# Optimization experiments

Measured on AMD Instinct MI355X. Metric: run time of the kernel, lower is better.

The kernel has to match this reference:

```python
import jax, jax.numpy as jnp
import numpy as np

B, NQ, NC, D, H, HD, FF, RB = 2, 512, 2048, 768, 12, 64, 3072, 64
EPS = 1e-5


def setup_inputs() -> dict:
    key = jax.random.key(0)
    ks = jax.random.split(key, 20)
    def n(k, shape, s=0.02):
        return jax.random.normal(k, shape, jnp.float32) * s
    return dict(
        query_state=n(ks[0], (B, NQ, D), 1.0),
        context_k=n(ks[1], (B, NC, D), 1.0),
        context_v=n(ks[2], (B, NC, D), 1.0),
        query_coords=jax.random.uniform(ks[3], (B, NQ, 2), jnp.float32),
        context_coords=jax.random.uniform(ks[4], (B, NC, 2), jnp.float32),
        sn_g=jnp.ones(D), sn_b=jnp.zeros(D),
        wqkv=n(ks[5], (D, 3 * D)), bqkv=jnp.zeros(3 * D),
        wo_s=n(ks[6], (D, D)), bo_s=jnp.zeros(D),
        cn_g=jnp.ones(D), cn_b=jnp.zeros(D),
        wq=n(ks[7], (D, D)), bq=jnp.zeros(D),
        wk=n(ks[8], (D, D)), bk=jnp.zeros(D),
        wv=n(ks[9], (D, D)), bv=jnp.zeros(D),
        wo_c=n(ks[10], (D, D)), bo_c=jnp.zeros(D),
        rb_w1=n(ks[11], (2, RB), 0.5), rb_b1=jnp.zeros(RB),
        rb_w2=n(ks[12], (RB, H), 0.5), rb_b2=jnp.zeros(H),
        fn_g=jnp.ones(D), fn_b=jnp.zeros(D),
        fw1=n(ks[13], (D, FF)), fb1=jnp.zeros(FF),
        fw2=n(ks[14], (FF, D)), fb2=jnp.zeros(D),
    )


def _ln(x, g, b):
    m = x.mean(-1, keepdims=True)
    v = ((x - m) ** 2).mean(-1, keepdims=True)
    return (x - m) / jnp.sqrt(v + EPS) * g + b


def _heads(x):
    # (B, N, D) -> (B, H, N, HD)
    return x.reshape(x.shape[0], x.shape[1], H, HD).transpose(0, 2, 1, 3)


def reference(query_state, context_k, context_v, query_coords, context_coords,
              sn_g, sn_b, wqkv, bqkv, wo_s, bo_s,
              cn_g, cn_b, wq, bq, wk, bk, wv, bv, wo_c, bo_c,
              rb_w1, rb_b1, rb_w2, rb_b2,
              fn_g, fn_b, fw1, fb1, fw2, fb2):
    scale = HD ** -0.5
    x = query_state

    # ---- pre-norm self-attention (nn.MultiheadAttention equivalent) ----
    qn = _ln(x, sn_g, sn_b)
    qkv = qn @ wqkv + bqkv                      # (B, NQ, 3D)
    q, k, v = jnp.split(qkv, 3, axis=-1)
    q, k, v = _heads(q), _heads(k), _heads(v)   # (B, H, NQ, HD)
    a = jax.nn.softmax(jnp.einsum('bhqd,bhkd->bhqk', q, k) * scale, axis=-1)
    o = jnp.einsum('bhqk,bhkd->bhqd', a, v).transpose(0, 2, 1, 3).reshape(B, NQ, D)
    x = x + o @ wo_s + bo_s

    # ---- relative coordinate bias: MLP(delta) -> (B, H, NQ, NC) ----
    delta = query_coords[:, :, None, :] - context_coords[:, None, :, :]  # (B, NQ, NC, 2)
    bias = jax.nn.gelu(delta @ rb_w1 + rb_b1, approximate=False) @ rb_w2 + rb_b2
    bias = bias.transpose(0, 3, 1, 2)           # (B, H, NQ, NC)

    # ---- pre-norm cross-attention with bias ----
    qn = _ln(x, cn_g, cn_b)
    q = _heads(qn @ wq + bq)                    # (B, H, NQ, HD)
    k = _heads(context_k @ wk + bk)             # (B, H, NC, HD)
    v = _heads(context_v @ wv + bv)
    logits = jnp.einsum('bhqd,bhkd->bhqk', q, k) * scale + bias
    a = jax.nn.softmax(logits, axis=-1)
    o = jnp.einsum('bhqk,bhkd->bhqd', a, v).transpose(0, 2, 1, 3).reshape(B, NQ, D)
    x = x + o @ wo_c + bo_c

    # ---- pre-norm FFN ----
    h = jax.nn.gelu(_ln(x, fn_g, fn_b) @ fw1 + fb1, approximate=False)
    x = x + h @ fw2 + fb2
    return x
```

## Files before the change

kernel.cpp:

```cpp
#include <hip/hip_runtime.h>

#define B_ 2
#define NQ_ 512
#define NC_ 2048
#define D_ 768
#define H_ 12
#define HD_ 64
#define FF_ 3072
#define RB_ 64

typedef unsigned short u16;
typedef __attribute__((ext_vector_type(4))) unsigned short u16x4;
typedef __attribute__((ext_vector_type(8))) short short8;
typedef __attribute__((ext_vector_type(4))) float f32x4;
typedef __attribute__((ext_vector_type(2))) float f32x2;

__device__ __forceinline__ float bf2f(u16 u) {
    unsigned int i = ((unsigned int)u) << 16;
    float f; __builtin_memcpy(&f, &i, 4); return f;
}
__device__ __forceinline__ u16 f2bf(float f) {
    unsigned int i; __builtin_memcpy(&i, &f, 4);
    unsigned int r = i + 0x7FFFu + ((i >> 16) & 1u);
    return (u16)(r >> 16);
}
__device__ __forceinline__ float gelu_f(float x) {
    return 0.5f * x * (1.f + erff(x * 0.70710678118654752f));
}
__device__ __forceinline__ float wsum(float v) {
    v += __shfl_xor(v, 32); v += __shfl_xor(v, 16); v += __shfl_xor(v, 8);
    v += __shfl_xor(v, 4);  v += __shfl_xor(v, 2);  v += __shfl_xor(v, 1);
    return v;
}
__device__ __forceinline__ void gload_lds16(const void* g, void* l) {
    __builtin_amdgcn_global_load_lds((const __attribute__((address_space(1))) void*)g,
                                     (__attribute__((address_space(3))) void*)l, 16, 0, 0);
}

__device__ __forceinline__ void wtrans_body(const float* __restrict__ in, u16* __restrict__ out,
                                            int K, int N, int bx, int by, int tid) {
    __shared__ float t[32][33];
    int n0 = bx * 32, k0 = by * 32;
    int tx = tid & 31, ty = tid >> 5;
#pragma unroll
    for (int r = 0; r < 4; ++r)
        t[ty + r * 8][tx] = in[(long)(k0 + ty + r * 8) * N + n0 + tx];
    __syncthreads();
#pragma unroll
    for (int r = 0; r < 4; ++r)
        out[(long)(n0 + ty + r * 8) * K + k0 + tx] = f2bf(t[tx][ty + r * 8]);
}

__global__ __launch_bounds__(256) void wtrans(const float* __restrict__ in, u16* __restrict__ out,
                                              int K, int N) {
    wtrans_body(in, out, K, N, blockIdx.x, blockIdx.y, threadIdx.x);
}

__global__ __launch_bounds__(256) void wtrans5(const float* i0, const float* i1, const float* i2,
                                               const float* i3, const float* i4,
                                               u16* o0, u16* o1, u16* o2, u16* o3, u16* o4) {
    const float* in; u16* out;
    switch (blockIdx.z) {
        case 0: in = i0; out = o0; break;
        case 1: in = i1; out = o1; break;
        case 2: in = i2; out = o2; break;
        case 3: in = i3; out = o3; break;
        default: in = i4; out = o4; break;
    }
    wtrans_body(in, out, 768, 768, blockIdx.x, blockIdx.y, threadIdx.x);
}

__global__ __launch_bounds__(256) void cvtk2(const float* __restrict__ inA, u16* __restrict__ outA,
                                             const float* __restrict__ inB, u16* __restrict__ outB, int n4) {
    int i = blockIdx.x * 256 + threadIdx.x;
    const float* in = blockIdx.y ? inB : inA;
    u16* out = blockIdx.y ? outB : outA;
    if (i < n4) {
        float4 v = ((const float4*)in)[i];
        u16x4 o; o.x = f2bf(v.x); o.y = f2bf(v.y); o.z = f2bf(v.z); o.w = f2bf(v.w);
        ((u16x4*)out)[i] = o;
    }
}

__global__ __launch_bounds__(256) void ln_k(const float* __restrict__ x, const float* __restrict__ g,
                                            const float* __restrict__ bta, u16* __restrict__ out) {
    int row = blockIdx.x, t = threadIdx.x;
    const float* xr = x + (long)row * D_;
    float a0 = xr[t], a1 = xr[t + 256], a2 = xr[t + 512];
    float s = a0 + a1 + a2, s2 = a0 * a0 + a1 * a1 + a2 * a2;
    s = wsum(s); s2 = wsum(s2);
    __shared__ float rb[8];
    int lane = t & 63, wid = t >> 6;
    if (!lane) { rb[wid] = s; rb[wid + 4] = s2; }
    __syncthreads();
    float S = rb[0] + rb[1] + rb[2] + rb[3];
    float S2 = rb[4] + rb[5] + rb[6] + rb[7];
    float mean = S * (1.f / D_);
    float var = S2 * (1.f / D_) - mean * mean;
    float rstd = rsqrtf(var + 1e-5f);
    u16* orow = out + (long)row * D_;
    orow[t]       = f2bf((a0 - mean) * rstd * g[t]       + bta[t]);
    orow[t + 256] = f2bf((a1 - mean) * rstd * g[t + 256] + bta[t + 256]);
    orow[t + 512] = f2bf((a2 - mean) * rstd * g[t + 512] + bta[t + 512]);
}

__global__ __launch_bounds__(256) void bias_mlp3(
    const float* __restrict__ qcoord, const float* __restrict__ ccoord,
    const float* __restrict__ w1, const float* __restrict__ b1,
    const float* __restrict__ w2, const float* __restrict__ b2,
    u16* __restrict__ out) {
    __shared__ float s1[192];
    __shared__ float sw2[RB_ * H_];
    __shared__ float2 sc[256];
    __shared__ u16 sb[12 * 264];
    int tid = threadIdx.x;
    int b = blockIdx.z, q = blockIdx.y, c0 = blockIdx.x * 256;
    if (tid < 64) { s1[tid] = w1[tid]; s1[64 + tid] = w1[64 + tid]; s1[128 + tid] = b1[tid]; }
    for (int i = tid; i < RB_ * H_; i += 256) sw2[i] = w2[i];
    sc[tid] = ((const float2*)ccoord)[b * NC_ + c0 + tid];
    __syncthreads();
    int lane = tid & 63, wid = tid >> 6;
    int h = lane & 15, g4 = lane >> 4;
    int j0 = g4 * 8;
    f32x2 wx[8], wy[8], bb[8];
#pragma unroll
    for (int p = 0; p < 4; ++p) {
        wx[p]     = (f32x2){s1[j0 + 2 * p],       s1[j0 + 2 * p + 1]};
        wy[p]     = (f32x2){s1[64 + j0 + 2 * p],  s1[64 + j0 + 2 * p + 1]};
        bb[p]     = (f32x2){s1[128 + j0 + 2 * p], s1[128 + j0 + 2 * p + 1]};
        wx[4 + p] = (f32x2){s1[32 + j0 + 2 * p],  s1[32 + j0 + 2 * p + 1]};
        wy[4 + p] = (f32x2){s1[96 + j0 + 2 * p],  s1[96 + j0 + 2 * p + 1]};
        bb[4 + p] = (f32x2){s1[160 + j0 + 2 * p], s1[160 + j0 + 2 * p + 1]};
    }
    short8 vb0, vb1;
#pragma unroll
    for (int u = 0; u < 8; ++u) {
        vb0[u] = (h < 12) ? (short)f2bf(sw2[(j0 + u) * H_ + h]) : (short)0;
        vb1[u] = (h < 12) ? (short)f2bf(sw2[(32 + j0 + u) * H_ + h]) : (short)0;
    }
    float qx = qcoord[(b * NQ_ + q) * 2], qy = qcoord[(b * NQ_ + q) * 2 + 1];
    float b2v = (h < 12) ? b2[h] : 0.f;
#pragma unroll
    for (int it = 0; it < 4; ++it) {
        int ci = wid * 64 + it * 16 + h;
        float2 cc = sc[ci];
        float dx = qx - cc.x, dy = qy - cc.y;
        unsigned int pk[8];
#pragma unroll
        for (int p = 0; p < 8; ++p) {
            f32x2 pre = dx * wx[p] + bb[p];
            pre = dy * wy[p] + pre;
            f32x2 t = pre * pre;
            f32x2 a = 1.5957691f + 0.07135482f * t;
            f32x2 uu = pre * a;
            f32x2 e; e.x = __expf(uu.x); e.y = __expf(uu.y);
            e = e + 1.0f;
            f32x2 r; r.x = __builtin_amdgcn_rcpf(e.x); r.y = __builtin_amdgcn_rcpf(e.y);
            f32x2 g = pre - pre * r;
            pk[p] = __builtin_amdgcn_perm(__builtin_bit_cast(unsigned int, g.y),
                                          __builtin_bit_cast(unsigned int, g.x), 0x07060302u);
        }
        uint4 d0 = {pk[0], pk[1], pk[2], pk[3]};
        uint4 d1 = {pk[4], pk[5], pk[6], pk[7]};
        short8 a0 = __builtin_bit_cast(short8, d0);
        short8 a1 = __builtin_bit_cast(short8, d1);
        f32x4 acc = {};
        acc = __builtin_amdgcn_mfma_f32_16x16x32_bf16(a0, vb0, acc, 0, 0, 0);
        acc = __builtin_amdgcn_mfma_f32_16x16x32_bf16(a1, vb1, acc, 0, 0, 0);
        if (h < 12) {
#pragma unroll
            for (int r = 0; r < 4; ++r) {
                int loc = wid * 64 + it * 16 + g4 * 4 + r;
                sb[h * 264 + loc] = f2bf(acc[r] + b2v);
            }
        }
    }
    __syncthreads();
    for (int i = tid; i < 12 * 128; i += 256) {
        int row = i >> 7, cp = (i & 127) * 2;
        unsigned int pv = *(const unsigned int*)(sb + row * 264 + cp);
        *(unsigned int*)(out + (((long)(b * H_ + row) * NQ_ + q) * NC_ + c0 + cp)) = pv;
    }
}

__global__ __launch_bounds__(256) void vtrans(const u16* __restrict__ in, u16* __restrict__ out,
                                              int NCt, int ldin, int bdiv, long sIb, long sIh) {
    __shared__ u16 t[32][33];
    int z = blockIdx.z, zb = z / bdiv, zh = z % bdiv;
    const u16* ib = in + zb * sIb + zh * sIh;
    int c0 = blockIdx.x * 32, d0 = blockIdx.y * 32;
    int tx = threadIdx.x & 31, ty = threadIdx.x >> 5;
#pragma unroll
    for (int r = 0; r < 4; ++r)
        t[ty + r * 8][tx] = ib[(long)(c0 + ty + r * 8) * ldin + d0 + tx];
    __syncthreads();
#pragma unroll
    for (int r = 0; r < 4; ++r)
        out[(long)z * 64 * NCt + (long)(d0 + ty + r * 8) * NCt + c0 + tx] = t[tx][ty + r * 8];
}

template <int NCT, bool HASBIAS>
__global__ __launch_bounds__(64) void fattn(
    const u16* __restrict__ Qb, const u16* __restrict__ Kb, const u16* __restrict__ Vtb,
    const u16* __restrict__ Bias, u16* __restrict__ Ob, int ldq, int ldk) {
    __shared__ u16 kl[2][128 * 64];
    __shared__ u16 vl[64 * 128];
    __shared__ u16 pl[16 * 128];
    const int lane = threadIdx.x;
    const int h16 = lane & 15, g4 = lane >> 4;
    const int hh = blockIdx.y, b = blockIdx.z, q0 = blockIdx.x * 16;
    const u16* Qrow = Qb + (long)(b * NQ_ + q0 + h16) * ldq + hh * 64;
    short8 qf0 = *(const short8*)(Qrow + g4 * 8);
    short8 qf1 = *(const short8*)(Qrow + 32 + g4 * 8);
    const u16* Kbase = Kb + (long)b * NCT * ldk + hh * 64;
    const u16* Vtbase = Vtb + (long)(b * H_ + hh) * 64 * NCT;
    const u16* Bbase = Bias ? Bias + ((long)(b * H_ + hh) * NQ_ + q0) * NCT : nullptr;

    auto stageK = [&](int buf, int c0) {
#pragma unroll
        for (int i = 0; i < 16; ++i) {
            int ch = i * 64 + lane;
            int row = ch >> 3, col2 = (ch & 7) * 16;
            int scol2 = col2 ^ ((row & 7) << 4);
            gload_lds16(Kbase + (long)(c0 + row) * ldk + (scol2 >> 1), &kl[buf][ch * 8]);
        }
    };
    auto stageV = [&](int c0) {
#pragma unroll
        for (int i = 0; i < 16; ++i) {
            int ch = i * 64 + lane;
            int row = ch >> 4, col2 = (ch & 15) * 16;
            int scol2 = col2 ^ ((row & 15) << 4);
            gload_lds16(Vtbase + (long)row * NCT + c0 + (scol2 >> 1), &vl[ch * 8]);
        }
    };

    float m0[4] = {-1e30f, -1e30f, -1e30f, -1e30f};
    float l0[4] = {0.f, 0.f, 0.f, 0.f};
    f32x4 oacc[4] = {};
    constexpr int T = NCT / 128;
    stageK(0, 0);
    for (int t = 0; t < T; ++t) {
        const int c0 = t * 128, cur = t & 1;
        asm volatile("s_waitcnt lgkmcnt(0)" ::: "memory");
        stageV(c0);
        float bv[8][4];
        if (HASBIAS) {
#pragma unroll
            for (int r = 0; r < 4; ++r)
#pragma unroll
                for (int n = 0; n < 8; ++n)
                    bv[n][r] = bf2f(Bbase[(long)(g4 * 4 + r) * NCT + c0 + n * 16 + h16]);
        }
        if (t + 1 < T) stageK(cur ^ 1, c0 + 128);
        if (HASBIAS) {
            asm volatile("s_waitcnt vmcnt(48)" ::: "memory");
        } else {
            if (t + 1 < T) asm volatile("s_waitcnt vmcnt(32)" ::: "memory");
            else           asm volatile("s_waitcnt vmcnt(16)" ::: "memory");
        }
        f32x4 sacc[8] = {};
        const u16* klc = kl[cur];
#pragma unroll
        for (int n = 0; n < 8; ++n) {
            int row = n * 16 + h16, swz = (row & 7) << 4;
#pragma unroll
            for (int ks = 0; ks < 2; ++ks) {
                short8 kf = *(const short8*)((const char*)klc + row * 128 + ((ks * 64 + g4 * 16) ^ swz));
                sacc[n] = __builtin_amdgcn_mfma_f32_16x16x32_bf16(ks ? qf1 : qf0, kf, sacc[n], 0, 0, 0);
            }
        }
        if (t + 1 < T) asm volatile("s_waitcnt vmcnt(16)" ::: "memory");
        else           asm volatile("s_waitcnt vmcnt(0)" ::: "memory");
        float cr[4];
#pragma unroll
        for (int r = 0; r < 4; ++r) {
            float mx = -1e30f;
#pragma unroll
            for (int n = 0; n < 8; ++n) {
                float s = sacc[n][r] * 0.125f;
                if (HASBIAS) s += bv[n][r];
                sacc[n][r] = s; mx = fmaxf(mx, s);
            }
            mx = fmaxf(mx, __shfl_xor(mx, 1)); mx = fmaxf(mx, __shfl_xor(mx, 2));
            mx = fmaxf(mx, __shfl_xor(mx, 4)); mx = fmaxf(mx, __shfl_xor(mx, 8));
            float mn = fmaxf(m0[r], mx);
            cr[r] = __expf(m0[r] - mn); m0[r] = mn;
            float sum = 0.f;
#pragma unroll
            for (int n = 0; n < 8; ++n) {
                float p = __expf(sacc[n][r] - mn); sacc[n][r] = p; sum += p;
            }
            sum += __shfl_xor(sum, 1); sum += __shfl_xor(sum, 2);
            sum += __shfl_xor(sum, 4); sum += __shfl_xor(sum, 8);
            l0[r] = l0[r] * cr[r] + sum;
        }
#pragma unroll
        for (int n = 0; n < 8; ++n)
#pragma unroll
            for (int r = 0; r < 4; ++r) {
                int q = g4 * 4 + r, c = n * 16 + h16;
                *(u16*)((char*)pl + q * 256 + ((c * 2) ^ (q << 4))) =
                    (u16)(__builtin_bit_cast(unsigned int, sacc[n][r]) >> 16);
            }
#pragma unroll
        for (int d = 0; d < 4; ++d) {
            f32x4 o = oacc[d];
            o[0] *= cr[0]; o[1] *= cr[1]; o[2] *= cr[2]; o[3] *= cr[3];
            oacc[d] = o;
        }
        short8 pf[4];
#pragma unroll
        for (int ks = 0; ks < 4; ++ks)
            pf[ks] = *(const short8*)((const char*)pl + h16 * 256 + ((ks * 64 + g4 * 16) ^ (h16 << 4)));
#pragma unroll
        for (int d = 0; d < 4; ++d) {
            int row = d * 16 + h16, swzv = (row & 15) << 4;
#pragma unroll
            for (int ks = 0; ks < 4; ++ks) {
                short8 vf = *(const short8*)((const char*)vl + row * 256 + ((ks * 64 + g4 * 16) ^ swzv));
                oacc[d] = __builtin_amdgcn_mfma_f32_16x16x32_bf16(pf[ks], vf, oacc[d], 0, 0, 0);
            }
        }
    }
    float inv[4];
#pragma unroll
    for (int r = 0; r < 4; ++r) inv[r] = 1.f / l0[r];
    u16* Orow = Ob + (long)(b * NQ_ + q0) * D_ + hh * 64;
#pragma unroll
    for (int d = 0; d < 4; ++d)
#pragma unroll
        for (int r = 0; r < 4; ++r)
            Orow[(long)(g4 * 4 + r) * D_ + d * 16 + h16] = f2bf(oacc[d][r] * inv[r]);
}

template <int T, int S>
__global__ __launch_bounds__(256) void fattn4(
    const u16* __restrict__ Qb, const u16* __restrict__ Kb, const u16* __restrict__ Vtb,
    const u16* __restrict__ Bias, float* __restrict__ Part,
    int ldq, int ldk, int ldv, int NCT) {
    __shared__ u16 kl[2][128 * 64];
    __shared__ u16 vl[64 * 128];
    __shared__ u16 bl[4][16 * 128];
    __shared__ u16 pl[4][16 * 128];
    const int tid = threadIdx.x, lane = tid & 63, wid = tid >> 6;
    const int h16 = lane & 15, g4 = lane >> 4;
    const int qb = blockIdx.x, hh = blockIdx.y;
    const int b = blockIdx.z / S, s = blockIdx.z % S;
    const int q0w = qb * 64 + wid * 16;
    const int cb = s * (T * 128);
    const u16* Qrow = Qb + (long)(b * NQ_ + q0w + h16) * ldq + hh * 64;
    short8 qf0 = *(const short8*)(Qrow + g4 * 8);
    short8 qf1 = *(const short8*)(Qrow + 32 + g4 * 8);
    const u16* Kbase = Kb + (long)b * NCT * ldk + hh * 64;
    const u16* Vtbase = Vtb + (long)(b * H_ + hh) * 64 * ldv;
    const u16* Bbase = Bias + ((long)(b * H_ + hh) * NQ_ + q0w) * NCT;
    u16* mypl = pl[wid];
    const u16* mybl = bl[wid];

    auto stageK = [&](int buf, int c0) {
#pragma unroll
        for (int i = 0; i < 4; ++i) {
            int ch = wid * 256 + i * 64 + lane;
            int row = ch >> 3, col2 = (ch & 7) * 16;
            int scol2 = col2 ^ ((row & 7) << 4);
            gload_lds16(Kbase + (long)(c0 + row) * ldk + (scol2 >> 1), &kl[buf][ch * 8]);
        }
    };
    auto stageV = [&](int c0) {
#pragma unroll
        for (int i = 0; i < 4; ++i) {
            int ch = wid * 256 + i * 64 + lane;
            int row = ch >> 4, col2 = (ch & 15) * 16;
            int scol2 = col2 ^ ((row & 15) << 4);
            gload_lds16(Vtbase + (long)row * ldv + c0 + (scol2 >> 1), &vl[ch * 8]);
        }
    };
    auto stageB = [&](int c0) {
#pragma unroll
        for (int i = 0; i < 4; ++i) {
            int ch = i * 64 + lane;
            int row = ch >> 4, col8 = ch & 15;
            int scol8 = col8 ^ (row & 7);
            gload_lds16(Bbase + (long)row * NCT + c0 + scol8 * 8, &bl[wid][ch * 8]);
        }
    };

    float m0[4] = {-1e30f, -1e30f, -1e30f, -1e30f};
    float l0[4] = {0.f, 0.f, 0.f, 0.f};
    f32x4 oacc[4] = {};
    stageK(0, cb);
    for (int t = 0; t < T; ++t) {
        const int c0 = cb + t * 128, cur = t & 1;
        if (t > 0) {
            asm volatile("s_waitcnt lgkmcnt(0)" ::: "memory");
            __builtin_amdgcn_sched_barrier(0);
            __builtin_amdgcn_s_barrier();
        }
        stageV(c0);
        stageB(c0);
        if (t + 1 < T) stageK(cur ^ 1, c0 + 128);
        if (t + 1 < T) asm volatile("s_waitcnt vmcnt(12)" ::: "memory");
        else           asm volatile("s_waitcnt vmcnt(8)" ::: "memory");
        __builtin_amdgcn_s_barrier();
        f32x4 sacc[8] = {};
        const u16* klc = kl[cur];
#pragma unroll
        for (int n = 0; n < 8; ++n) {
            int row = n * 16 + h16, swz = (row & 7) << 4;
#pragma unroll
            for (int ks = 0; ks < 2; ++ks) {
                short8 kf = *(const short8*)((const char*)klc + row * 128 + ((ks * 64 + g4 * 16) ^ swz));
                sacc[n] = __builtin_amdgcn_mfma_f32_16x16x32_bf16(ks ? qf1 : qf0, kf, sacc[n], 0, 0, 0);
            }
        }
        if (t + 1 < T) asm volatile("s_waitcnt vmcnt(4)" ::: "memory");
        else           asm volatile("s_waitcnt vmcnt(0)" ::: "memory");
        __builtin_amdgcn_s_barrier();
        float cr[4];
#pragma unroll
        for (int r = 0; r < 4; ++r) {
            int q = g4 * 4 + r;
            float mx = -1e30f;
#pragma unroll
            for (int n = 0; n < 8; ++n) {
                float bvv = bf2f(*(const u16*)((const char*)mybl + q * 256 +
                                 (((n * 16 + h16) * 2) ^ ((q & 7) << 4))));
                float sv = sacc[n][r] * 0.125f + bvv;
                sacc[n][r] = sv; mx = fmaxf(mx, sv);
            }
            mx = fmaxf(mx, __shfl_xor(mx, 1)); mx = fmaxf(mx, __shfl_xor(mx, 2));
            mx = fmaxf(mx, __shfl_xor(mx, 4)); mx = fmaxf(mx, __shfl_xor(mx, 8));
            float mn = fmaxf(m0[r], mx);
            cr[r] = __expf(m0[r] - mn); m0[r] = mn;
            float sum = 0.f;
#pragma unroll
            for (int n = 0; n < 8; ++n) {
                float p = __expf(sacc[n][r] - mn); sacc[n][r] = p; sum += p;
            }
            sum += __shfl_xor(sum, 1); sum += __shfl_xor(sum, 2);
            sum += __shfl_xor(sum, 4); sum += __shfl_xor(sum, 8);
            l0[r] = l0[r] * cr[r] + sum;
        }
#pragma unroll
        for (int n = 0; n < 8; ++n)
#pragma unroll
            for (int r = 0; r < 4; ++r) {
                int q = g4 * 4 + r, c = n * 16 + h16;
                *(u16*)((char*)mypl + q * 256 + ((c * 2) ^ (q << 4))) =
                    (u16)(__builtin_bit_cast(unsigned int, sacc[n][r]) >> 16);
            }
#pragma unroll
        for (int d = 0; d < 4; ++d) {
            f32x4 o = oacc[d];
            o[0] *= cr[0]; o[1] *= cr[1]; o[2] *= cr[2]; o[3] *= cr[3];
            oacc[d] = o;
        }
        short8 pf[4];
#pragma unroll
        for (int ks = 0; ks < 4; ++ks)
            pf[ks] = *(const short8*)((const char*)mypl + h16 * 256 + ((ks * 64 + g4 * 16) ^ (h16 << 4)));
#pragma unroll
        for (int d = 0; d < 4; ++d) {
            int row = d * 16 + h16, swzv = (row & 15) << 4;
#pragma unroll
            for (int ks = 0; ks < 4; ++ks) {
                short8 vf = *(const short8*)((const char*)vl + row * 256 + ((ks * 64 + g4 * 16) ^ swzv));
                oacc[d] = __builtin_amdgcn_mfma_f32_16x16x32_bf16(pf[ks], vf, oacc[d], 0, 0, 0);
            }
        }
    }
    float* P = Part + ((((long)(b * H_ + hh) * 32 + qb * 4 + wid) * S + s) * 1088);
#pragma unroll
    for (int d = 0; d < 4; ++d)
#pragma unroll
        for (int r = 0; r < 4; ++r)
            P[(g4 * 4 + r) * 64 + d * 16 + h16] = oacc[d][r];
    if (h16 == 0) {
#pragma unroll
        for (int r = 0; r < 4; ++r) {
            P[1024 + g4 * 4 + r] = m0[r];
            P[1056 + g4 * 4 + r] = l0[r];
        }
    }
}

__global__ __launch_bounds__(64) void fcomb(const float* __restrict__ Part, u16* __restrict__ Ob) {
    int q16 = blockIdx.x, hh = blockIdx.y, b = blockIdx.z, lane = threadIdx.x;
    const float* base = Part + (((long)(b * H_ + hh) * 32 + q16) * 4) * 1088;
#pragma unroll 4
    for (int q = 0; q < 16; ++q) {
        float m0 = base[1024 + q],        m1 = base[1088 + 1024 + q];
        float m2 = base[2176 + 1024 + q], m3 = base[3264 + 1024 + q];
        float M = fmaxf(fmaxf(m0, m1), fmaxf(m2, m3));
        float w0 = __expf(m0 - M), w1 = __expf(m1 - M);
        float w2 = __expf(m2 - M), w3 = __expf(m3 - M);
        float L = w0 * base[1056 + q] + w1 * base[1088 + 1056 + q] +
                  w2 * base[2176 + 1056 + q] + w3 * base[3264 + 1056 + q];
        float o = w0 * base[q * 64 + lane] + w1 * base[1088 + q * 64 + lane] +
                  w2 * base[2176 + q * 64 + lane] + w3 * base[3264 + q * 64 + lane];
        Ob[(long)(b * NQ_ + q16 * 16 + q) * D_ + hh * 64 + lane] = f2bf(o * (1.f / L));
    }
}

enum { EP_BIAS = 0, EP_SCALE = 1, EP_SCALEACC = 2, EP_RES = 3, EP_GELU = 4 };

template <int BM, int BN, int EPI>
__global__ __launch_bounds__(256) void gemm_bt(
    const u16* __restrict__ A, const u16* __restrict__ B, void* __restrict__ Cv,
    const float* __restrict__ bias, const float* __restrict__ res,
    int M, int N, int K, int lda, int ldb, int ldc,
    int bdiv, long sAb, long sAh, long sBb, long sBh, long sCb, long sCh,
    float scale) {
    constexpr int BK = 64;
    __shared__ u16 lA[BM * BK];
    __shared__ u16 lB[BN * BK];
    const int z = blockIdx.z;
    const int zb = z / bdiv, zh = z % bdiv;
    const u16* Ab = A + zb * sAb + zh * sAh;
    const u16* Bb = B + zb * sBb + zh * sBh;
    const int bm = blockIdx.y * BM;
    const int bn = blockIdx.x * BN;
    const int tid = threadIdx.x;
    const int lane = tid & 63, wid = tid >> 6;
    const int wm = (wid >> 1) * (BM / 2);
    const int wn = (wid & 1) * (BN / 2);
    constexpr int FM = BM / 32, FN = BN / 32;
    f32x4 acc[FM][FN] = {};
    const int lrow = lane & 15, lk = (lane >> 4) * 8;

    for (int kb = 0; kb < K; kb += BK) {
#pragma unroll
        for (int i = 0; i < (BM * 8) / 256; ++i) {
            int ch = tid + i * 256;
            int r = ch >> 3, c = ch & 7;
            gload_lds16(Ab + (long)(bm + r) * lda + kb + c * 8, lA + ch * 8);
        }
#pragma unroll
        for (int i = 0; i < (BN * 8) / 256; ++i) {
            int ch = tid + i * 256;
            int r = ch >> 3, c = ch & 7;
            gload_lds16(Bb + (long)(bn + r) * ldb + kb + c * 8, lB + ch * 8);
        }
        __syncthreads();
#pragma unroll
        for (int ks = 0; ks < 2; ++ks) {
            short8 af[FM], bfr[FN];
#pragma unroll
            for (int i = 0; i < FM; ++i)
                af[i] = *(const short8*)(lA + (wm + i * 16 + lrow) * BK + ks * 32 + lk);
#pragma unroll
            for (int j = 0; j < FN; ++j)
                bfr[j] = *(const short8*)(lB + (wn + j * 16 + lrow) * BK + ks * 32 + lk);
#pragma unroll
            for (int i = 0; i < FM; ++i)
#pragma unroll
                for (int j = 0; j < FN; ++j)
                    acc[i][j] = __builtin_amdgcn_mfma_f32_16x16x32_bf16(af[i], bfr[j], acc[i][j], 0, 0, 0);
        }
        __syncthreads();
    }

    long coff = zb * sCb + zh * sCh;
#pragma unroll
    for (int i = 0; i < FM; ++i) {
#pragma unroll
        for (int j = 0; j < FN; ++j) {
#pragma unroll
            for (int r = 0; r < 4; ++r) {
                int row = bm + wm + i * 16 + (lane >> 4) * 4 + r;
                int col = bn + wn + j * 16 + (lane & 15);
                long idx = coff + (long)row * ldc + col;
                float v = acc[i][j][r];
                if (EPI == EP_SCALE) {
                    ((u16*)Cv)[idx] = f2bf(v * scale);
                } else if (EPI == EP_RES) {
                    float tt = v + (bias ? bias[col] : 0.f);
                    ((float*)Cv)[idx] = res[idx] + tt;
                } else if (EPI == EP_GELU) {
                    float tt = v + (bias ? bias[col] : 0.f);
                    ((u16*)Cv)[idx] = f2bf(gelu_f(tt));
                } else {
                    float tt = v + (bias ? bias[col] : 0.f);
                    ((u16*)Cv)[idx] = f2bf(tt);
                }
            }
        }
    }
}

extern "C" void kernel_launch(void* const* d_in, const int* in_sizes, int n_in,
                              void* d_out, int out_size, void* d_ws, size_t ws_size,
                              hipStream_t stream) {
    const float* x_in   = (const float*)d_in[0];
    const float* ctx_k  = (const float*)d_in[1];
    const float* ctx_v  = (const float*)d_in[2];
    const float* qcoord = (const float*)d_in[3];
    const float* ccoord = (const float*)d_in[4];
    const float* sn_g   = (const float*)d_in[5];
    const float* sn_b   = (const float*)d_in[6];
    const float* wqkv   = (const float*)d_in[7];
    const float* bqkv   = (const float*)d_in[8];
    const float* wo_s   = (const float*)d_in[9];
    const float* bo_s   = (const float*)d_in[10];
    const float* cn_g   = (const float*)d_in[11];
    const float* cn_b   = (const float*)d_in[12];
    const float* wq     = (const float*)d_in[13];
    const float* bq     = (const float*)d_in[14];
    const float* wk     = (const float*)d_in[15];
    const float* bk     = (const float*)d_in[16];
    const float* wv     = (const float*)d_in[17];
    const float* bv     = (const float*)d_in[18];
    const float* wo_c   = (const float*)d_in[19];
    const float* bo_c   = (const float*)d_in[20];
    const float* rb_w1  = (const float*)d_in[21];
    const float* rb_b1  = (const float*)d_in[22];
    const float* rb_w2  = (const float*)d_in[23];
    const float* rb_b2  = (const float*)d_in[24];
    const float* fn_g   = (const float*)d_in[25];
    const float* fn_b   = (const float*)d_in[26];
    const float* fw1    = (const float*)d_in[27];
    const float* fb1    = (const float*)d_in[28];
    const float* fw2    = (const float*)d_in[29];
    const float* fb2    = (const float*)d_in[30];

    char* ws = (char*)d_ws;
    size_t off = 0;
    auto alloc = [&](size_t bytes) -> void* {
        void* p = ws + off; off += (bytes + 255) & ~(size_t)255; return p;
    };
    u16* wT_qkv = (u16*)alloc((size_t)2304 * 768 * 2);
    u16* wT_os  = (u16*)alloc((size_t)768 * 768 * 2);
    u16* wT_q   = (u16*)alloc((size_t)768 * 768 * 2);
    u16* wT_k   = (u16*)alloc((size_t)768 * 768 * 2);
    u16* wT_v   = (u16*)alloc((size_t)768 * 768 * 2);
    u16* wT_oc  = (u16*)alloc((size_t)768 * 768 * 2);
    u16* wT_f1  = (u16*)alloc((size_t)3072 * 768 * 2);
    u16* wT_f2  = (u16*)alloc((size_t)768 * 3072 * 2);
    u16* ckb    = (u16*)alloc((size_t)B_ * NC_ * D_ * 2);
    u16* cvb    = (u16*)alloc((size_t)B_ * NC_ * D_ * 2);
    u16* xln    = (u16*)alloc((size_t)1024 * 768 * 2);
    u16* qkv    = (u16*)alloc((size_t)1024 * 2304 * 2);
    u16* vts    = (u16*)alloc((size_t)24 * 64 * 512 * 2);
    u16* oatt   = (u16*)alloc((size_t)1024 * 768 * 2);
    float* x1   = (float*)alloc((size_t)1024 * 768 * 4);
    u16* xln2   = (u16*)alloc((size_t)1024 * 768 * 2);
    u16* qc     = (u16*)alloc((size_t)1024 * 768 * 2);
    u16* kc     = (u16*)alloc((size_t)4096 * 768 * 2);
    u16* vc     = (u16*)alloc((size_t)4096 * 768 * 2);
    u16* clog   = (u16*)alloc((size_t)24 * 512 * 2048 * 2);
    u16* vtc    = (u16*)alloc((size_t)24 * 64 * 2048 * 2);
    u16* oc2    = (u16*)alloc((size_t)1024 * 768 * 2);
    float* x2   = (float*)alloc((size_t)1024 * 768 * 4);
    u16* xln3   = (u16*)alloc((size_t)1024 * 768 * 2);
    u16* ffh    = (u16*)alloc((size_t)1024 * 3072 * 2);
    float* part = (float*)alloc((size_t)2 * H_ * 32 * 4 * 1088 * 4);
    (void)ws_size; (void)in_sizes; (void)n_in; (void)out_size;

    wtrans<<<dim3(2304 / 32, 768 / 32), 256, 0, stream>>>(wqkv, wT_qkv, 768, 2304);
    wtrans5<<<dim3(24, 24, 5), 256, 0, stream>>>(wo_s, wq, wk, wv, wo_c,
                                                 wT_os, wT_q, wT_k, wT_v, wT_oc);
    wtrans<<<dim3(3072 / 32, 768 / 32), 256, 0, stream>>>(fw1, wT_f1, 768, 3072);
    wtrans<<<dim3(768 / 32, 3072 / 32), 256, 0, stream>>>(fw2, wT_f2, 3072, 768);
    cvtk2<<<dim3(B_ * NC_ * D_ / 4 / 256, 2), 256, 0, stream>>>(ctx_k, ckb, ctx_v, cvb, B_ * NC_ * D_ / 4);

    ln_k<<<1024, 256, 0, stream>>>(x_in, sn_g, sn_b, xln);
    gemm_bt<64, 128, EP_BIAS><<<dim3(2304 / 128, 1024 / 64, 1), 256, 0, stream>>>(
        xln, wT_qkv, qkv, bqkv, nullptr, 1024, 2304, 768, 768, 768, 2304,
        1, 0, 0, 0, 0, 0, 0, 1.f);
    bias_mlp3<<<dim3(NC_ / 256, NQ_, B_), 256, 0, stream>>>(qcoord, ccoord, rb_w1, rb_b1, rb_w2, rb_b2, clog);
    vtrans<<<dim3(512 / 32, 2, 24), 256, 0, stream>>>(qkv + 1536, vts, 512, 2304, 12, (long)512 * 2304, 64);
    fattn<512, false><<<dim3(NQ_ / 16, H_, B_), 64, 0, stream>>>(
        qkv, qkv + 768, vts, nullptr, oatt, 2304, 2304);
    gemm_bt<32, 64, EP_RES><<<dim3(768 / 64, 1024 / 32, 1), 256, 0, stream>>>(
        oatt, wT_os, x1, bo_s, x_in, 1024, 768, 768, 768, 768, 768,
        1, 0, 0, 0, 0, 0, 0, 1.f);

    ln_k<<<1024, 256, 0, stream>>>(x1, cn_g, cn_b, xln2);
    gemm_bt<32, 64, EP_BIAS><<<dim3(768 / 64, 1024 / 32, 1), 256, 0, stream>>>(
        xln2, wT_q, qc, bq, nullptr, 1024, 768, 768, 768, 768, 768,
        1, 0, 0, 0, 0, 0, 0, 1.f);
    gemm_bt<64, 128, EP_BIAS><<<dim3(768 / 128, 4096 / 64, 1), 256, 0, stream>>>(
        ckb, wT_k, kc, bk, nullptr, 4096, 768, 768, 768, 768, 768,
        1, 0, 0, 0, 0, 0, 0, 1.f);
    gemm_bt<64, 128, EP_BIAS><<<dim3(768 / 128, 4096 / 64, 1), 256, 0, stream>>>(
        cvb, wT_v, vc, bv, nullptr, 4096, 768, 768, 768, 768, 768,
        1, 0, 0, 0, 0, 0, 0, 1.f);
    vtrans<<<dim3(2048 / 32, 2, 24), 256, 0, stream>>>(vc, vtc, 2048, 768, 12, (long)2048 * 768, 64);
    fattn4<4, 4><<<dim3(8, H_, B_ * 4), 256, 0, stream>>>(
        qc, kc, vtc, clog, part, 768, 768, 2048, 2048);
    fcomb<<<dim3(32, H_, B_), 64, 0, stream>>>(part, oc2);
    gemm_bt<32, 64, EP_RES><<<dim3(768 / 64, 1024 / 32, 1), 256, 0, stream>>>(
        oc2, wT_oc, x2, bo_c, x1, 1024, 768, 768, 768, 768, 768,
        1, 0, 0, 0, 0, 0, 0, 1.f);

    ln_k<<<1024, 256, 0, stream>>>(x2, fn_g, fn_b, xln3);
    gemm_bt<64, 128, EP_GELU><<<dim3(3072 / 128, 1024 / 64, 1), 256, 0, stream>>>(
        xln3, wT_f1, ffh, fb1, nullptr, 1024, 3072, 768, 768, 768, 3072,
        1, 0, 0, 0, 0, 0, 0, 1.f);
    gemm_bt<32, 64, EP_RES><<<dim3(768 / 64, 1024 / 32, 1), 256, 0, stream>>>(
        ffh, wT_f2, (float*)d_out, fb2, x2, 1024, 768, 3072, 3072, 3072, 768,
        1, 0, 0, 0, 0, 0, 0, 1.f);
}
```

Measured before the change: 280.1 us.

## Batch bias MLP over four queries, use exp2 softmax, shrink cross-attn tile

The bias MLP kernel now handles four query rows per block, so weight and coordinate staging is shared across them. Its output is pre-scaled by log2(e), which lets both attention kernels use native exp2 with a folded scale constant. The cross-attention kernel moves from 128-column to 64-column KV tiles with twice the iterations, which lowers LDS use and may raise occupancy. s_setprio hints wrap the MFMA sections, and the dead bias path is removed from the self-attention kernel.

```diff
diff --git a/kernel.cpp b/kernel.cpp
--- a/kernel.cpp
+++ b/kernel.cpp
@@ -14,6 +14,8 @@
 typedef __attribute__((ext_vector_type(8))) short short8;
 typedef __attribute__((ext_vector_type(4))) float f32x4;
 typedef __attribute__((ext_vector_type(2))) float f32x2;
+
+#define SCL2 0.18033688f
 
 __device__ __forceinline__ float bf2f(u16 u) {
     unsigned int i = ((unsigned int)u) << 16;
@@ -104,7 +106,7 @@
     orow[t + 512] = f2bf((a2 - mean) * rstd * g[t + 512] + bta[t + 512]);
 }
 
-__global__ __launch_bounds__(256) void bias_mlp3(
+__global__ __launch_bounds__(256) void bias_mlp4(
     const float* __restrict__ qcoord, const float* __restrict__ ccoord,
     const float* __restrict__ w1, const float* __restrict__ b1,
     const float* __restrict__ w2, const float* __restrict__ b2,
@@ -112,9 +114,9 @@
     __shared__ float s1[192];
     __shared__ float sw2[RB_ * H_];
     __shared__ float2 sc[256];
-    __shared__ u16 sb[12 * 264];
+    __shared__ u16 sb[4][12 * 264];
     int tid = threadIdx.x;
-    int b = blockIdx.z, q = blockIdx.y, c0 = blockIdx.x * 256;
+    int b = blockIdx.z, q0 = blockIdx.y * 4, c0 = blockIdx.x * 256;
     if (tid < 64) { s1[tid] = w1[tid]; s1[64 + tid] = w1[64 + tid]; s1[128 + tid] = b1[tid]; }
     for (int i = tid; i < RB_ * H_; i += 256) sw2[i] = w2[i];
     sc[tid] = ((const float2*)ccoord)[b * NC_ + c0 + tid];
@@ -138,48 +140,58 @@
         vb0[u] = (h < 12) ? (short)f2bf(sw2[(j0 + u) * H_ + h]) : (short)0;
         vb1[u] = (h < 12) ? (short)f2bf(sw2[(32 + j0 + u) * H_ + h]) : (short)0;
     }
-    float qx = qcoord[(b * NQ_ + q) * 2], qy = qcoord[(b * NQ_ + q) * 2 + 1];
+    float qx[4], qy[4];
+#pragma unroll
+    for (int qq = 0; qq < 4; ++qq) {
+        qx[qq] = qcoord[(b * NQ_ + q0 + qq) * 2];
+        qy[qq] = qcoord[(b * NQ_ + q0 + qq) * 2 + 1];
+    }
     float b2v = (h < 12) ? b2[h] : 0.f;
 #pragma unroll
-    for (int it = 0; it < 4; ++it) {
-        int ci = wid * 64 + it * 16 + h;
-        float2 cc = sc[ci];
-        float dx = qx - cc.x, dy = qy - cc.y;
-        unsigned int pk[8];
-#pragma unroll
-        for (int p = 0; p < 8; ++p) {
-            f32x2 pre = dx * wx[p] + bb[p];
-            pre = dy * wy[p] + pre;
-            f32x2 t = pre * pre;
-            f32x2 a = 1.5957691f + 0.07135482f * t;
-            f32x2 uu = pre * a;
-            f32x2 e; e.x = __expf(uu.x); e.y = __expf(uu.y);
-            e = e + 1.0f;
-            f32x2 r; r.x = __builtin_amdgcn_rcpf(e.x); r.y = __builtin_amdgcn_rcpf(e.y);
-            f32x2 g = pre - pre * r;
-            pk[p] = __builtin_amdgcn_perm(__builtin_bit_cast(unsigned int, g.y),
-                                          __builtin_bit_cast(unsigned int, g.x), 0x07060302u);
-        }
-        uint4 d0 = {pk[0], pk[1], pk[2], pk[3]};
-        uint4 d1 = {pk[4], pk[5], pk[6], pk[7]};
-        short8 a0 = __builtin_bit_cast(short8, d0);
-        short8 a1 = __builtin_bit_cast(short8, d1);
-        f32x4 acc = {};
-        acc = __builtin_amdgcn_mfma_f32_16x16x32_bf16(a0, vb0, acc, 0, 0, 0);
-        acc = __builtin_amdgcn_mfma_f32_16x16x32_bf16(a1, vb1, acc, 0, 0, 0);
-        if (h < 12) {
-#pragma unroll
-            for (int r = 0; r < 4; ++r) {
-                int loc = wid * 64 + it * 16 + g4 * 4 + r;
-                sb[h * 264 + loc] = f2bf(acc[r] + b2v);
+    for (int qq = 0; qq < 4; ++qq) {
+#pragma unroll
+        for (int it = 0; it < 4; ++it) {
+            int ci = wid * 64 + it * 16 + h;
+            float2 cc = sc[ci];
+            float dx = qx[qq] - cc.x, dy = qy[qq] - cc.y;
+            unsigned int pk[8];
+#pragma unroll
+            for (int p = 0; p < 8; ++p) {
+                f32x2 pre = dx * wx[p] + bb[p];
+                pre = dy * wy[p] + pre;
+                f32x2 t = pre * pre;
+                f32x2 a = 2.3022082f + 0.10294325f * t;
+                f32x2 uu = pre * a;
+                f32x2 e; e.x = __builtin_amdgcn_exp2f(uu.x); e.y = __builtin_amdgcn_exp2f(uu.y);
+                e = e + 1.0f;
+                f32x2 r; r.x = __builtin_amdgcn_rcpf(e.x); r.y = __builtin_amdgcn_rcpf(e.y);
+                f32x2 g = pre - pre * r;
+                pk[p] = __builtin_amdgcn_perm(__builtin_bit_cast(unsigned int, g.y),
+                                              __builtin_bit_cast(unsigned int, g.x), 0x07060302u);
+            }
+            uint4 d0 = {pk[0], pk[1], pk[2], pk[3]};
+            uint4 d1 = {pk[4], pk[5], pk[6], pk[7]};
+            short8 a0 = __builtin_bit_cast(short8, d0);
+            short8 a1 = __builtin_bit_cast(short8, d1);
+            f32x4 acc = {};
+            acc = __builtin_amdgcn_mfma_f32_16x16x32_bf16(a0, vb0, acc, 0, 0, 0);
+            acc = __builtin_amdgcn_mfma_f32_16x16x32_bf16(a1, vb1, acc, 0, 0, 0);
+            if (h < 12) {
+#pragma unroll
+                for (int r = 0; r < 4; ++r) {
+                    int loc = wid * 64 + it * 16 + g4 * 4 + r;
+                    sb[qq][h * 264 + loc] = f2bf((acc[r] + b2v) * 1.4426950f);
+                }
             }
         }
     }
     __syncthreads();
-    for (int i = tid; i < 12 * 128; i += 256) {
-        int row = i >> 7, cp = (i & 127) * 2;
-        unsigned int pv = *(const unsigned int*)(sb + row * 264 + cp);
-        *(unsigned int*)(out + (((long)(b * H_ + row) * NQ_ + q) * NC_ + c0 + cp)) = pv;
+    for (int i = tid; i < 12 * 4 * 128; i += 256) {
+        int row = i >> 9;
+        int rem = i & 511;
+        int qq = rem >> 7, cp = (rem & 127) * 2;
+        unsigned int pv = *(const unsigned int*)(sb[qq] + row * 264 + cp);
+        *(unsigned int*)(out + (((long)(b * H_ + row) * NQ_ + q0 + qq) * NC_ + c0 + cp)) = pv;
     }
 }
 
@@ -214,7 +226,6 @@
     short8 qf1 = *(const short8*)(Qrow + 32 + g4 * 8);
     const u16* Kbase = Kb + (long)b * NCT * ldk + hh * 64;
     const u16* Vtbase = Vtb + (long)(b * H_ + hh) * 64 * NCT;
-    const u16* Bbase = Bias ? Bias + ((long)(b * H_ + hh) * NQ_ + q0) * NCT : nullptr;
 
     auto stageK = [&](int buf, int c0) {
 #pragma unroll
@@ -244,23 +255,12 @@
         const int c0 = t * 128, cur = t & 1;
         asm volatile("s_waitcnt lgkmcnt(0)" ::: "memory");
         stageV(c0);
-        float bv[8][4];
-        if (HASBIAS) {
-#pragma unroll
-            for (int r = 0; r < 4; ++r)
-#pragma unroll
-                for (int n = 0; n < 8; ++n)
-                    bv[n][r] = bf2f(Bbase[(long)(g4 * 4 + r) * NCT + c0 + n * 16 + h16]);
-        }
         if (t + 1 < T) stageK(cur ^ 1, c0 + 128);
-        if (HASBIAS) {
-            asm volatile("s_waitcnt vmcnt(48)" ::: "memory");
-        } else {
-            if (t + 1 < T) asm volatile("s_waitcnt vmcnt(32)" ::: "memory");
-            else           asm volatile("s_waitcnt vmcnt(16)" ::: "memory");
-        }
+        if (t + 1 < T) asm volatile("s_waitcnt vmcnt(32)" ::: "memory");
+        else           asm volatile("s_waitcnt vmcnt(16)" ::: "memory");
         f32x4 sacc[8] = {};
         const u16* klc = kl[cur];
+        __builtin_amdgcn_s_setprio(1);
 #pragma unroll
         for (int n = 0; n < 8; ++n) {
             int row = n * 16 + h16, swz = (row & 7) << 4;
@@ -270,6 +270,7 @@
                 sacc[n] = __builtin_amdgcn_mfma_f32_16x16x32_bf16(ks ? qf1 : qf0, kf, sacc[n], 0, 0, 0);
             }
         }
+        __builtin_amdgcn_s_setprio(0);
         if (t + 1 < T) asm volatile("s_waitcnt vmcnt(16)" ::: "memory");
         else           asm volatile("s_waitcnt vmcnt(0)" ::: "memory");
         float cr[4];
@@ -278,18 +279,17 @@
             float mx = -1e30f;
 #pragma unroll
             for (int n = 0; n < 8; ++n) {
-                float s = sacc[n][r] * 0.125f;
-                if (HASBIAS) s += bv[n][r];
+                float s = sacc[n][r] * SCL2;
                 sacc[n][r] = s; mx = fmaxf(mx, s);
             }
             mx = fmaxf(mx, __shfl_xor(mx, 1)); mx = fmaxf(mx, __shfl_xor(mx, 2));
             mx = fmaxf(mx, __shfl_xor(mx, 4)); mx = fmaxf(mx, __shfl_xor(mx, 8));
             float mn = fmaxf(m0[r], mx);
-            cr[r] = __expf(m0[r] - mn); m0[r] = mn;
+            cr[r] = __builtin_amdgcn_exp2f(m0[r] - mn); m0[r] = mn;
             float sum = 0.f;
 #pragma unroll
             for (int n = 0; n < 8; ++n) {
-                float p = __expf(sacc[n][r] - mn); sacc[n][r] = p; sum += p;
+                float p = __builtin_amdgcn_exp2f(sacc[n][r] - mn); sacc[n][r] = p; sum += p;
             }
             sum += __shfl_xor(sum, 1); sum += __shfl_xor(sum, 2);
             sum += __shfl_xor(sum, 4); sum += __shfl_xor(sum, 8);
@@ -313,6 +313,7 @@
 #pragma unroll
         for (int ks = 0; ks < 4; ++ks)
             pf[ks] = *(const short8*)((const char*)pl + h16 * 256 + ((ks * 64 + g4 * 16) ^ (h16 << 4)));
+        __builtin_amdgcn_s_setprio(1);
 #pragma unroll
         for (int d = 0; d < 4; ++d) {
             int row = d * 16 + h16, swzv = (row & 15) << 4;
@@ -322,6 +323,7 @@
                 oacc[d] = __builtin_amdgcn_mfma_f32_16x16x32_bf16(pf[ks], vf, oacc[d], 0, 0, 0);
             }
         }
+        __builtin_amdgcn_s_setprio(0);
     }
     float inv[4];
 #pragma unroll
@@ -339,16 +341,16 @@
     const u16* __restrict__ Qb, const u16* __restrict__ Kb, const u16* __restrict__ Vtb,
     const u16* __restrict__ Bias, float* __restrict__ Part,
     int ldq, int ldk, int ldv, int NCT) {
-    __shared__ u16 kl[2][128 * 64];
-    __shared__ u16 vl[64 * 128];
-    __shared__ u16 bl[4][16 * 128];
-    __shared__ u16 pl[4][16 * 128];
+    __shared__ u16 kl[2][64 * 64];
+    __shared__ u16 vl[64 * 64];
+    __shared__ u16 bl[4][16 * 64];
+    __shared__ u16 pl[4][16 * 64];
     const int tid = threadIdx.x, lane = tid & 63, wid = tid >> 6;
     const int h16 = lane & 15, g4 = lane >> 4;
     const int qb = blockIdx.x, hh = blockIdx.y;
     const int b = blockIdx.z / S, s = blockIdx.z % S;
     const int q0w = qb * 64 + wid * 16;
-    const int cb = s * (T * 128);
+    const int cb = s * (T * 64);
     const u16* Qrow = Qb + (long)(b * NQ_ + q0w + h16) * ldq + hh * 64;
     short8 qf0 = *(const short8*)(Qrow + g4 * 8);
     short8 qf1 = *(const short8*)(Qrow + 32 + g4 * 8);
@@ -360,8 +362,8 @@
 
     auto stageK = [&](int buf, int c0) {
 #pragma unroll
-        for (int i = 0; i < 4; ++i) {
-            int ch = wid * 256 + i * 64 + lane;
+        for (int i = 0; i < 2; ++i) {
+            int ch = wid * 128 + i * 64 + lane;
             int row = ch >> 3, col2 = (ch & 7) * 16;
             int scol2 = col2 ^ ((row & 7) << 4);
             gload_lds16(Kbase + (long)(c0 + row) * ldk + (scol2 >> 1), &kl[buf][ch * 8]);
@@ -369,20 +371,20 @@
     };
     auto stageV = [&](int c0) {
 #pragma unroll
-        for (int i = 0; i < 4; ++i) {
-            int ch = wid * 256 + i * 64 + lane;
-            int row = ch >> 4, col2 = (ch & 15) * 16;
-            int scol2 = col2 ^ ((row & 15) << 4);
+        for (int i = 0; i < 2; ++i) {
+            int ch = wid * 128 + i * 64 + lane;
+            int row = ch >> 3, col2 = (ch & 7) * 16;
+            int scol2 = col2 ^ ((row & 7) << 4);
             gload_lds16(Vtbase + (long)row * ldv + c0 + (scol2 >> 1), &vl[ch * 8]);
         }
     };
     auto stageB = [&](int c0) {
 #pragma unroll
-        for (int i = 0; i < 4; ++i) {
+        for (int i = 0; i < 2; ++i) {
             int ch = i * 64 + lane;
-            int row = ch >> 4, col8 = ch & 15;
-            int scol8 = col8 ^ (row & 7);
-            gload_lds16(Bbase + (long)row * NCT + c0 + scol8 * 8, &bl[wid][ch * 8]);
+            int row = ch >> 3, c16 = ch & 7;
+            int sc16 = c16 ^ (row & 7);
+            gload_lds16(Bbase + (long)row * NCT + c0 + sc16 * 8, &bl[wid][ch * 8]);
         }
     };
 
@@ -391,7 +393,7 @@
     f32x4 oacc[4] = {};
     stageK(0, cb);
     for (int t = 0; t < T; ++t) {
-        const int c0 = cb + t * 128, cur = t & 1;
+        const int c0 = cb + t * 64, cur = t & 1;
         if (t > 0) {
             asm volatile("s_waitcnt lgkmcnt(0)" ::: "memory");
             __builtin_amdgcn_sched_barrier(0);
@@ -399,14 +401,15 @@
         }
         stageV(c0);
         stageB(c0);
-        if (t + 1 < T) stageK(cur ^ 1, c0 + 128);
-        if (t + 1 < T) asm volatile("s_waitcnt vmcnt(12)" ::: "memory");
-        else           asm volatile("s_waitcnt vmcnt(8)" ::: "memory");
+        if (t + 1 < T) stageK(cur ^ 1, c0 + 64);
+        if (t + 1 < T) asm volatile("s_waitcnt vmcnt(6)" ::: "memory");
+        else           asm volatile("s_waitcnt vmcnt(4)" ::: "memory");
         __builtin_amdgcn_s_barrier();
-        f32x4 sacc[8] = {};
+        f32x4 sacc[4] = {};
         const u16* klc = kl[cur];
-#pragma unroll
-        for (int n = 0; n < 8; ++n) {
+        __builtin_amdgcn_s_setprio(1);
+#pragma unroll
+        for (int n = 0; n < 4; ++n) {
             int row = n * 16 + h16, swz = (row & 7) << 4;
 #pragma unroll
             for (int ks = 0; ks < 2; ++ks) {
@@ -414,7 +417,8 @@
                 sacc[n] = __builtin_amdgcn_mfma_f32_16x16x32_bf16(ks ? qf1 : qf0, kf, sacc[n], 0, 0, 0);
             }
         }
-        if (t + 1 < T) asm volatile("s_waitcnt vmcnt(4)" ::: "memory");
+        __builtin_amdgcn_s_setprio(0);
+        if (t + 1 < T) asm volatile("s_waitcnt vmcnt(2)" ::: "memory");
         else           asm volatile("s_waitcnt vmcnt(0)" ::: "memory");
         __builtin_amdgcn_s_barrier();
         float cr[4];
@@ -423,31 +427,31 @@
             int q = g4 * 4 + r;
             float mx = -1e30f;
 #pragma unroll
-            for (int n = 0; n < 8; ++n) {
-                float bvv = bf2f(*(const u16*)((const char*)mybl + q * 256 +
+            for (int n = 0; n < 4; ++n) {
+                float bvv = bf2f(*(const u16*)((const char*)mybl + q * 128 +
                                  (((n * 16 + h16) * 2) ^ ((q & 7) << 4))));
-                float sv = sacc[n][r] * 0.125f + bvv;
+                float sv = sacc[n][r] * SCL2 + bvv;
                 sacc[n][r] = sv; mx = fmaxf(mx, sv);
             }
             mx = fmaxf(mx, __shfl_xor(mx, 1)); mx = fmaxf(mx, __shfl_xor(mx, 2));
             mx = fmaxf(mx, __shfl_xor(mx, 4)); mx = fmaxf(mx, __shfl_xor(mx, 8));
             float mn = fmaxf(m0[r], mx);
-            cr[r] = __expf(m0[r] - mn); m0[r] = mn;
+            cr[r] = __builtin_amdgcn_exp2f(m0[r] - mn); m0[r] = mn;
             float sum = 0.f;
 #pragma unroll
-            for (int n = 0; n < 8; ++n) {
-                float p = __expf(sacc[n][r] - mn); sacc[n][r] = p; sum += p;
+            for (int n = 0; n < 4; ++n) {
+                float p = __builtin_amdgcn_exp2f(sacc[n][r] - mn); sacc[n][r] = p; sum += p;
             }
             sum += __shfl_xor(sum, 1); sum += __shfl_xor(sum, 2);
             sum += __shfl_xor(sum, 4); sum += __shfl_xor(sum, 8);
             l0[r] = l0[r] * cr[r] + sum;
         }
 #pragma unroll
-        for (int n = 0; n < 8; ++n)
+        for (int n = 0; n < 4; ++n)
 #pragma unroll
             for (int r = 0; r < 4; ++r) {
                 int q = g4 * 4 + r, c = n * 16 + h16;
-                *(u16*)((char*)mypl + q * 256 + ((c * 2) ^ (q << 4))) =
+                *(u16*)((char*)mypl + q * 128 + ((c * 2) ^ ((q & 7) << 4))) =
                     (u16)(__builtin_bit_cast(unsigned int, sacc[n][r]) >> 16);
             }
 #pragma unroll
@@ -456,19 +460,21 @@
             o[0] *= cr[0]; o[1] *= cr[1]; o[2] *= cr[2]; o[3] *= cr[3];
             oacc[d] = o;
         }
-        short8 pf[4];
-#pragma unroll
-        for (int ks = 0; ks < 4; ++ks)
-            pf[ks] = *(const short8*)((const char*)mypl + h16 * 256 + ((ks * 64 + g4 * 16) ^ (h16 << 4)));
+        short8 pf[2];
+#pragma unroll
+        for (int ks = 0; ks < 2; ++ks)
+            pf[ks] = *(const short8*)((const char*)mypl + h16 * 128 + ((ks * 64 + g4 * 16) ^ ((h16 & 7) << 4)));
+        __builtin_amdgcn_s_setprio(1);
 #pragma unroll
         for (int d = 0; d < 4; ++d) {
-            int row = d * 16 + h16, swzv = (row & 15) << 4;
-#pragma unroll
-            for (int ks = 0; ks < 4; ++ks) {
-                short8 vf = *(const short8*)((const char*)vl + row * 256 + ((ks * 64 + g4 * 16) ^ swzv));
+            int row = d * 16 + h16, swzv = (row & 7) << 4;
+#pragma unroll
+            for (int ks = 0; ks < 2; ++ks) {
+                short8 vf = *(const short8*)((const char*)vl + row * 128 + ((ks * 64 + g4 * 16) ^ swzv));
                 oacc[d] = __builtin_amdgcn_mfma_f32_16x16x32_bf16(pf[ks], vf, oacc[d], 0, 0, 0);
             }
         }
+        __builtin_amdgcn_s_setprio(0);
     }
     float* P = Part + ((((long)(b * H_ + hh) * 32 + qb * 4 + wid) * S + s) * 1088);
 #pragma unroll
@@ -493,8 +499,8 @@
         float m0 = base[1024 + q],        m1 = base[1088 + 1024 + q];
         float m2 = base[2176 + 1024 + q], m3 = base[3264 + 1024 + q];
         float M = fmaxf(fmaxf(m0, m1), fmaxf(m2, m3));
-        float w0 = __expf(m0 - M), w1 = __expf(m1 - M);
-        float w2 = __expf(m2 - M), w3 = __expf(m3 - M);
+        float w0 = __builtin_amdgcn_exp2f(m0 - M), w1 = __builtin_amdgcn_exp2f(m1 - M);
+        float w2 = __builtin_amdgcn_exp2f(m2 - M), w3 = __builtin_amdgcn_exp2f(m3 - M);
         float L = w0 * base[1056 + q] + w1 * base[1088 + 1056 + q] +
                   w2 * base[2176 + 1056 + q] + w3 * base[3264 + 1056 + q];
         float o = w0 * base[q * 64 + lane] + w1 * base[1088 + q * 64 + lane] +
@@ -668,7 +674,7 @@
     gemm_bt<64, 128, EP_BIAS><<<dim3(2304 / 128, 1024 / 64, 1), 256, 0, stream>>>(
         xln, wT_qkv, qkv, bqkv, nullptr, 1024, 2304, 768, 768, 768, 2304,
         1, 0, 0, 0, 0, 0, 0, 1.f);
-    bias_mlp3<<<dim3(NC_ / 256, NQ_, B_), 256, 0, stream>>>(qcoord, ccoord, rb_w1, rb_b1, rb_w2, rb_b2, clog);
+    bias_mlp4<<<dim3(NC_ / 256, NQ_ / 4, B_), 256, 0, stream>>>(qcoord, ccoord, rb_w1, rb_b1, rb_w2, rb_b2, clog);
     vtrans<<<dim3(512 / 32, 2, 24), 256, 0, stream>>>(qkv + 1536, vts, 512, 2304, 12, (long)512 * 2304, 64);
     fattn<512, false><<<dim3(NQ_ / 16, H_, B_), 64, 0, stream>>>(
         qkv, qkv + 768, vts, nullptr, oatt, 2304, 2304);
@@ -687,7 +693,7 @@
         cvb, wT_v, vc, bv, nullptr, 4096, 768, 768, 768, 768, 768,
         1, 0, 0, 0, 0, 0, 0, 1.f);
     vtrans<<<dim3(2048 / 32, 2, 24), 256, 0, stream>>>(vc, vtc, 2048, 768, 12, (long)2048 * 768, 64);
-    fattn4<4, 4><<<dim3(8, H_, B_ * 4), 256, 0, stream>>>(
+    fattn4<8, 4><<<dim3(8, H_, B_ * 4), 256, 0, stream>>>(
         qc, kc, vtc, clog, part, 768, 768, 2048, 2048);
     fcomb<<<dim3(32, H_, B_), 64, 0, stream>>>(part, oc2);
     gemm_bt<32, 64, EP_RES><<<dim3(768 / 64, 1024 / 32, 1), 256, 0, stream>>>(
```

Result: no change. 275.3 us (-1.7%).
